# Optimization experiments

Measured on AMD Instinct MI355X. Metric: run time of the kernel, lower is better.

Reference implementation:

```python
import jax, jax.numpy as jnp
import numpy as np

N = 131072          # flattened ray-sample points
C = 32              # output_coordinate_dim per plane
BASE = 128          # base grid resolution
SCALES = [1, 2, 4]  # multiscale_res multipliers
HID = 256           # ResBlock / CondMLP hidden width
OUT = 16            # decoder output dim (geo features)
COMBS = [(0, 1), (0, 2), (1, 2)]  # itertools.combinations(range(3), 2)


def setup_inputs() -> dict:
    key = jax.random.key(0)
    ks = iter(jax.random.split(key, 64))
    inp = {}
    inp['pts'] = jax.random.uniform(next(ks), (N, 3), dtype=jnp.float32)
    inp['aabb'] = jnp.asarray([[0.0, 0.0, 0.0], [1.0, 1.0, 1.0]], dtype=jnp.float32)
    # 9 plane grids: 3 scales x 3 coordinate combinations, uniform in [0.1, 0.5)
    for s, mult in enumerate(SCALES):
        r = BASE * mult
        for ci in range(3):
            inp[f'plane_{s}_{ci}'] = jax.random.uniform(
                next(ks), (C, r, r), dtype=jnp.float32, minval=0.1, maxval=0.5)
    feat_dim = C * len(SCALES)  # concat across scales -> 96
    def lin(k, fin, fout):
        bound = 1.0 / np.sqrt(fin)
        kw, kb = jax.random.split(k)
        w = jax.random.uniform(kw, (fin, fout), dtype=jnp.float32, minval=-bound, maxval=bound)
        b = jax.random.uniform(kb, (fout,), dtype=jnp.float32, minval=-bound, maxval=bound)
        return w, b
    inp['l0_w'], inp['l0_b'] = lin(next(ks), feat_dim, HID)
    # 3 ResBlocks x 3 linears (lz, l1, l2), all 256x256 -> stacked
    rw, rb = [], []
    for _ in range(9):
        w, b = lin(next(ks), HID, HID)
        rw.append(w); rb.append(b)
    inp['res_w'] = jnp.stack(rw).reshape(3, 3, HID, HID)
    inp['res_b'] = jnp.stack(rb).reshape(3, 3, HID)
    inp['l1_w'], inp['l1_b'] = lin(next(ks), HID, OUT)
    return inp


def _bilinear(plane, xy):
    # plane: [C, H, W]; xy: [N, 2] in [-1, 1]; x -> W axis, y -> H axis
    # (F.grid_sample, align_corners=True; border clamp == zeros pad since pts in-bounds)
    Cc, H, W = plane.shape
    x = (xy[:, 0] + 1.0) * 0.5 * (W - 1)
    y = (xy[:, 1] + 1.0) * 0.5 * (H - 1)
    x0 = jnp.clip(jnp.floor(x), 0, W - 2).astype(jnp.int32)
    y0 = jnp.clip(jnp.floor(y), 0, H - 2).astype(jnp.int32)
    x1, y1 = x0 + 1, y0 + 1
    wx = (x - x0)[None, :]
    wy = (y - y0)[None, :]
    v = (plane[:, y0, x0] * (1 - wx) * (1 - wy)
         + plane[:, y0, x1] * wx * (1 - wy)
         + plane[:, y1, x0] * (1 - wx) * wy
         + plane[:, y1, x1] * wx * wy)          # [C, N]
    return v.T                                   # [N, C]


def _interp_ms(xn, planes):
    # planes: list of 3 scales, each a list of 3 [C,H,W] grids
    feats = []
    for scale_planes in planes:
        interp = 1.0
        for plane, (c0, c1) in zip(scale_planes, COMBS):
            xy = jnp.stack([xn[:, c0], xn[:, c1]], axis=-1)
            interp = interp * _bilinear(plane, xy)  # hadamard across planes
        feats.append(interp)
    return jnp.concatenate(feats, axis=-1)          # [N, C*num_scales]


def _cond_mlp(f, l0_w, l0_b, res_w, res_b, l1_w, l1_b):
    x = f @ l0_w + l0_b
    for i in range(3):
        z = jax.nn.relu(x @ res_w[i, 0] + res_b[i, 0])
        res = x + z
        x = jax.nn.relu(res @ res_w[i, 1] + res_b[i, 1])
        x = jax.nn.relu(x @ res_w[i, 2] + res_b[i, 2]) + res
    return jax.nn.sigmoid(x @ l1_w + l1_b)


def reference(pts, aabb,
              plane_0_0, plane_0_1, plane_0_2,
              plane_1_0, plane_1_1, plane_1_2,
              plane_2_0, plane_2_1, plane_2_2,
              l0_w, l0_b, res_w, res_b, l1_w, l1_b):
    xn = (pts - aabb[0]) * (2.0 / (aabb[1] - aabb[0])) - 1.0  # normalize_aabb
    planes = [[plane_0_0, plane_0_1, plane_0_2],
              [plane_1_0, plane_1_1, plane_1_2],
              [plane_2_0, plane_2_1, plane_2_2]]
    feats = _interp_ms(xn, planes)                            # [N, 96]
    return _cond_mlp(feats, l0_w, l0_b, res_w, res_b, l1_w, l1_b)  # [N, 16]
```

## Files before the change

### kernel.cpp

```cpp
#include <hip/hip_runtime.h>

typedef unsigned short u16;
typedef unsigned int u32;
typedef __attribute__((ext_vector_type(2))) unsigned int u32x2;
typedef __attribute__((ext_vector_type(8))) short short8;
typedef __attribute__((ext_vector_type(8))) _Float16 half8;
typedef __attribute__((ext_vector_type(2))) __fp16 fp16x2;
typedef __attribute__((ext_vector_type(4))) float floatx4;

__device__ __forceinline__ u16 f2h(float f){ _Float16 h = (_Float16)f; return __builtin_bit_cast(u16, h); }
__device__ __forceinline__ u32 pkrtz(float a, float b){
  fp16x2 h = __builtin_amdgcn_cvt_pkrtz(a, b);
  return __builtin_bit_cast(u32, h);
}
__device__ __forceinline__ u32 pkmax0(u32 a){
  u32 d, z = 0;
  asm("v_pk_max_f16 %0, %1, %2" : "=v"(d) : "v"(a), "v"(z));
  return d;
}
__device__ __forceinline__ u32 pkadd(u32 a, u32 b){
  u32 d;
  asm("v_pk_add_f16 %0, %1, %2" : "=v"(d) : "v"(a), "v"(b));
  return d;
}

struct PlanePtrs { const void* p[9]; };
struct PtransArgs { const float* src[9]; u16* dst[9]; int blk0[10]; int HW[9]; };

__global__ void ptrans_all_kernel(PtransArgs a){
  __shared__ float tile[32][257];
  int bi = blockIdx.x;
  int i = 0;
  #pragma unroll
  for (int k = 1; k < 9; k++) if (bi >= a.blk0[k]) i = k;
  const float* src = a.src[i];
  u16* dst = a.dst[i];
  const int HW = a.HW[i];
  const int t = threadIdx.x;
  const size_t hw0 = (size_t)(bi - a.blk0[i]) * 256;
  #pragma unroll
  for (int c = 0; c < 32; c++) tile[c][t] = src[(size_t)c*HW + hw0 + t];
  __syncthreads();
  u32* d32 = (u32*)(dst + hw0*32);
  #pragma unroll
  for (int k = 0; k < 16; k++){
    int idx = k*512 + t*2;
    int j = idx >> 5, cc = idx & 31;
    u32 lo = f2h(tile[cc][j]);
    u32 hi = f2h(tile[cc+1][j]);
    d32[k*256 + t] = lo | (hi << 16);
  }
}

__device__ __forceinline__ void wconv_one(const float* src, u16* dst, int fin, int fout, int t){
  int per = fin * fout;
  int m = t / per, r = t - m*per;
  int KS = fin >> 5;
  int e = r & 7;
  int lane = (r >> 3) & 63;
  int fs = r >> 9;
  int ks = fs % KS, ft = fs / KS;
  int of = ft*16 + (lane & 15);
  int k  = ks*32 + (lane >> 4)*8 + e;
  dst[t] = f2h(src[(size_t)m*per + (size_t)k*fout + of]);
}
__global__ void wconv_all_kernel(const float* l0_w, const float* res_w, const float* l1_w,
                                 u16* l0T, u16* resT, u16* l1T){
  int t = blockIdx.x*256 + threadIdx.x;
  if (t < 24576){ wconv_one(l0_w, l0T, 96, 256, t); return; }
  t -= 24576;
  if (t < 589824){ wconv_one(res_w, resT, 256, 256, t); return; }
  t -= 589824;
  if (t < 4096){ wconv_one(l1_w, l1T, 256, 16, t); }
}

__global__ void interp_fb_kernel(const float* __restrict__ pts, const float* __restrict__ aabb,
                                 PlanePtrs pp, u16* __restrict__ feats, int N)
{
  int n = blockIdx.x*256 + threadIdx.x;
  if (n >= N) return;
  float xn[3];
  #pragma unroll
  for (int d=0; d<3; d++){
    float lo = aabb[d], hi = aabb[3+d];
    xn[d] = (pts[(size_t)n*3 + d] - lo) * (2.0f/(hi - lo)) - 1.0f;
  }
  const int c0s[3] = {0,0,1};
  const int c1s[3] = {1,2,2};
  #pragma unroll
  for (int s=0; s<3; s++){
    const int R = 128 << s;
    float prod[32];
    #pragma unroll
    for (int p=0; p<3; p++){
      float fx = (xn[c0s[p]] + 1.0f) * 0.5f * (float)(R-1);
      float fy = (xn[c1s[p]] + 1.0f) * 0.5f * (float)(R-1);
      float fx0 = fminf(fmaxf(floorf(fx), 0.0f), (float)(R-2));
      float fy0 = fminf(fmaxf(floorf(fy), 0.0f), (float)(R-2));
      int x0 = (int)fx0, y0 = (int)fy0;
      float wx = fx - fx0, wy = fy - fy0;
      float w00 = (1.0f-wx)*(1.0f-wy), w01 = wx*(1.0f-wy);
      float w10 = (1.0f-wx)*wy,        w11 = wx*wy;
      const size_t HW = (size_t)R*R;
      const float* b00f = (const float*)pp.p[s*3+p] + (size_t)y0*R + x0;
      #pragma unroll 4
      for (int c=0; c<32; c++){
        const float* q = b00f + (size_t)c*HW;
        float val = q[0]*w00 + q[1]*w01 + q[R]*w10 + q[R+1]*w11;
        prod[c] = (p == 0) ? val : prod[c]*val;
      }
    }
    #pragma unroll
    for (int vv=0; vv<4; vv++){
      short8 pk8;
      #pragma unroll
      for (int e=0; e<8; e++) pk8[e] = (short)f2h(prod[vv*8+e]);
      *(short8*)(feats + (size_t)n*96 + s*32 + vv*8) = pk8;
    }
  }
}

template<int KSTEPS>
__device__ __forceinline__ void mm_tile(const u16* X, const u16* __restrict__ WTs,
                                        int ftbase, int lane, const floatx4 binit[4],
                                        floatx4 acc[4][4])
{
  const int lr = lane & 15, lg = lane >> 4;
  #pragma unroll
  for (int rf=0; rf<4; rf++)
    #pragma unroll
    for (int cf=0; cf<4; cf++)
      acc[rf][cf] = binit[rf];
  #pragma unroll 1
  for (int ks=0; ks<KSTEPS; ks++){
    half8 w[4];
    #pragma unroll
    for (int rf=0; rf<4; rf++)
      w[rf] = *(const half8*)(WTs + ((size_t)((ftbase+rf)*KSTEPS + ks)*64 + lane)*8);
    half8 x[4];
    #pragma unroll
    for (int cf=0; cf<4; cf++){
      int pt = cf*16 + lr;
      int byt = (pt*512 + (ks*32 + lg*8)*2) ^ ((pt & 7) << 4);
      x[cf] = *(const half8*)((const char*)X + byt);
    }
    __builtin_amdgcn_s_setprio(1);
    #pragma unroll
    for (int rf=0; rf<4; rf++)
      #pragma unroll
      for (int cf=0; cf<4; cf++)
        acc[rf][cf] = __builtin_amdgcn_mfma_f32_16x16x32_f16(w[rf], x[cf], acc[rf][cf], 0, 0, 0);
    __builtin_amdgcn_s_setprio(0);
  }
}

__device__ __forceinline__ void load_binit(const float* b, int wb, int lg, floatx4* bi){
  #pragma unroll
  for (int rf=0; rf<4; rf++){
    float4 v = *(const float4*)(b + wb + rf*16 + lg*4);
    bi[rf] = (floatx4){v.x, v.y, v.z, v.w};
  }
}

template<bool GATHER>
__global__ __launch_bounds__(256, 3) void mlp_kernel(
    const float* __restrict__ pts, const float* __restrict__ aabb, PlanePtrs pp,
    const u16* __restrict__ feats,
    const u16* __restrict__ l0T, const u16* __restrict__ resT, const u16* __restrict__ l1T,
    const float* __restrict__ l0_b, const float* __restrict__ res_b, const float* __restrict__ l1_b,
    float* __restrict__ out)
{
  __shared__ u16 X[64*256];
  const int tid = threadIdx.x;
  const int wave = tid >> 6, lane = tid & 63;
  const int lr = lane & 15, lg = lane >> 4;
  const int n0 = blockIdx.x * 64;
  const int ftbase = wave * 4;
  const int wb = wave * 64;

  if constexpr (GATHER){
    const int pt = tid >> 2, v = tid & 3;
    const int n = n0 + pt;
    float xn[3];
    #pragma unroll
    for (int d=0; d<3; d++){
      float lo = aabb[d], hi = aabb[3+d];
      xn[d] = (pts[(size_t)n*3 + d] - lo) * (2.0f/(hi - lo)) - 1.0f;
    }
    const int c0s[3] = {0,0,1};
    const int c1s[3] = {1,2,2};
    #pragma unroll
    for (int s=0; s<3; s++){
      const int R = 128 << s;
      float prod[8];
      #pragma unroll
      for (int p=0; p<3; p++){
        float fx = (xn[c0s[p]] + 1.0f) * 0.5f * (float)(R-1);
        float fy = (xn[c1s[p]] + 1.0f) * 0.5f * (float)(R-1);
        float fx0 = fminf(fmaxf(floorf(fx), 0.0f), (float)(R-2));
        float fy0 = fminf(fmaxf(floorf(fy), 0.0f), (float)(R-2));
        int x0 = (int)fx0, y0 = (int)fy0;
        float wx = fx - fx0, wy = fy - fy0;
        float w00 = (1.0f-wx)*(1.0f-wy), w01 = wx*(1.0f-wy);
        float w10 = (1.0f-wx)*wy,        w11 = wx*wy;
        const u16* base = (const u16*)pp.p[s*3 + p];
        const u16* b00 = base + ((size_t)y0*R + x0)*32 + v*8;
        const u16* b10 = b00 + (size_t)R*32;
        half8 h00 = *(const half8*)b00;
        half8 h01 = *(const half8*)(b00 + 32);
        half8 h10 = *(const half8*)b10;
        half8 h11 = *(const half8*)(b10 + 32);
        #pragma unroll
        for (int e=0; e<8; e++){
          float val = (float)h00[e]*w00 + (float)h01[e]*w01 + (float)h10[e]*w10 + (float)h11[e]*w11;
          prod[e] = (p == 0) ? val : prod[e]*val;
        }
      }
      short8 pk8;
      #pragma unroll
      for (int e=0; e<8; e++) pk8[e] = (short)f2h(prod[e]);
      int byt = (pt*512 + (s*32 + v*8)*2) ^ ((pt & 7) << 4);
      *(short8*)((char*)X + byt) = pk8;
    }
  } else {
    #pragma unroll
    for (int i=0; i<3; i++){
      int id = tid + i*256;
      int row = id / 12, sub = id - row*12;
      short8 v = *(const short8*)(feats + (size_t)(n0+row)*96 + sub*8);
      int byt = (row*512 + sub*16) ^ ((row & 7) << 4);
      *(short8*)((char*)X + byt) = v;
    }
  }
  __syncthreads();

  floatx4 acc[4][4];
  floatx4 binit[4];
  u32 pk[4][4][2];

  load_binit(l0_b, wb, lg, binit);
  mm_tile<3>(X, l0T, ftbase, lane, binit, acc);
  __syncthreads();
  #pragma unroll
  for (int rf=0; rf<4; rf++){
    int fby = (wb + rf*16 + lg*4)*2;
    #pragma unroll
    for (int cf=0; cf<4; cf++){
      int pt = cf*16 + lr;
      u32 p0 = pkrtz(acc[rf][cf][0], acc[rf][cf][1]);
      u32 p1 = pkrtz(acc[rf][cf][2], acc[rf][cf][3]);
      pk[rf][cf][0] = p0; pk[rf][cf][1] = p1;
      int byt = (pt*512 + fby) ^ ((pt & 7) << 4);
      *(u32x2*)((char*)X + byt) = (u32x2){p0, p1};
    }
  }
  __syncthreads();

  for (int rb=0; rb<3; rb++){
    const u16* W0 = resT + (size_t)(rb*3+0)*65536;
    const u16* W1 = resT + (size_t)(rb*3+1)*65536;
    const u16* W2 = resT + (size_t)(rb*3+2)*65536;
    const float* b0 = res_b + (rb*3+0)*256;
    const float* b1 = res_b + (rb*3+1)*256;
    const float* b2 = res_b + (rb*3+2)*256;

    load_binit(b0, wb, lg, binit);
    mm_tile<8>(X, W0, ftbase, lane, binit, acc);
    __syncthreads();
    #pragma unroll
    for (int rf=0; rf<4; rf++){
      int fby = (wb + rf*16 + lg*4)*2;
      #pragma unroll
      for (int cf=0; cf<4; cf++){
        int pt = cf*16 + lr;
        u32 p0 = pkadd(pk[rf][cf][0], pkmax0(pkrtz(acc[rf][cf][0], acc[rf][cf][1])));
        u32 p1 = pkadd(pk[rf][cf][1], pkmax0(pkrtz(acc[rf][cf][2], acc[rf][cf][3])));
        pk[rf][cf][0] = p0; pk[rf][cf][1] = p1;
        int byt = (pt*512 + fby) ^ ((pt & 7) << 4);
        *(u32x2*)((char*)X + byt) = (u32x2){p0, p1};
      }
    }
    __syncthreads();

    load_binit(b1, wb, lg, binit);
    mm_tile<8>(X, W1, ftbase, lane, binit, acc);
    __syncthreads();
    #pragma unroll
    for (int rf=0; rf<4; rf++){
      int fby = (wb + rf*16 + lg*4)*2;
      #pragma unroll
      for (int cf=0; cf<4; cf++){
        int pt = cf*16 + lr;
        u32 p0 = pkmax0(pkrtz(acc[rf][cf][0], acc[rf][cf][1]));
        u32 p1 = pkmax0(pkrtz(acc[rf][cf][2], acc[rf][cf][3]));
        int byt = (pt*512 + fby) ^ ((pt & 7) << 4);
        *(u32x2*)((char*)X + byt) = (u32x2){p0, p1};
      }
    }
    __syncthreads();

    load_binit(b2, wb, lg, binit);
    mm_tile<8>(X, W2, ftbase, lane, binit, acc);
    __syncthreads();
    #pragma unroll
    for (int rf=0; rf<4; rf++){
      int fby = (wb + rf*16 + lg*4)*2;
      #pragma unroll
      for (int cf=0; cf<4; cf++){
        int pt = cf*16 + lr;
        u32 p0 = pkadd(pkmax0(pkrtz(acc[rf][cf][0], acc[rf][cf][1])), pk[rf][cf][0]);
        u32 p1 = pkadd(pkmax0(pkrtz(acc[rf][cf][2], acc[rf][cf][3])), pk[rf][cf][1]);
        pk[rf][cf][0] = p0; pk[rf][cf][1] = p1;
        int byt = (pt*512 + fby) ^ ((pt & 7) << 4);
        *(u32x2*)((char*)X + byt) = (u32x2){p0, p1};
      }
    }
    __syncthreads();
  }

  floatx4 accf;
  {
    float4 bo = *(const float4*)(l1_b + lg*4);
    accf = (floatx4){bo.x, bo.y, bo.z, bo.w};
  }
  #pragma unroll 1
  for (int ks=0; ks<8; ks++){
    int pt = wave*16 + lr;
    int byt = (pt*512 + (ks*32 + lg*8)*2) ^ ((pt&7)<<4);
    half8 x = *(const half8*)((const char*)X + byt);
    half8 w = *(const half8*)(l1T + ((size_t)ks*64 + lane)*8);
    accf = __builtin_amdgcn_mfma_f32_16x16x32_f16(w, x, accf, 0, 0, 0);
  }
  {
    float4 o;
    o.x = 1.0f / (1.0f + __expf(-accf[0]));
    o.y = 1.0f / (1.0f + __expf(-accf[1]));
    o.z = 1.0f / (1.0f + __expf(-accf[2]));
    o.w = 1.0f / (1.0f + __expf(-accf[3]));
    *(float4*)(out + (size_t)(n0 + wave*16 + lr)*16 + lg*4) = o;
  }
}

extern "C" void kernel_launch(void* const* d_in, const int* in_sizes, int n_in,
                              void* d_out, int out_size, void* d_ws, size_t ws_size,
                              hipStream_t stream)
{
  const float* pts  = (const float*)d_in[0];
  const float* aabb = (const float*)d_in[1];
  const float* l0_w = (const float*)d_in[11];
  const float* res_w= (const float*)d_in[13];
  const float* l1_w = (const float*)d_in[15];
  const float* l0_b = (const float*)d_in[12];
  const float* res_b= (const float*)d_in[14];
  const float* l1_b = (const float*)d_in[16];
  const int N = in_sizes[0] / 3;

  char* ws = (char*)d_ws;
  const size_t woff_l0  = 0;
  const size_t woff_res = 49152;
  const size_t woff_l1  = woff_res + 9*65536*2;
  const size_t foff     = woff_l1 + 8192;
  const size_t poff     = foff + (size_t)N*96*2;

  static const int HWs[3] = {128*128, 256*256, 512*512};
  size_t pel[9]; size_t tot = 0;
  for (int s=0;s<3;s++) for (int p=0;p<3;p++){ pel[s*3+p] = tot; tot += (size_t)HWs[s]*32; }

  const bool tr_mode = (ws_size >= poff + tot*2);

  wconv_all_kernel<<<(24576+589824+4096+255)/256, 256, 0, stream>>>(
      l0_w, res_w, l1_w, (u16*)(ws+woff_l0), (u16*)(ws+woff_res), (u16*)(ws+woff_l1));

  PlanePtrs pp;
  if (tr_mode){
    u16* pbase = (u16*)(ws + poff);
    PtransArgs pa;
    int b0 = 0;
    for (int i=0;i<9;i++){
      int s = i/3;
      pa.src[i] = (const float*)d_in[2+i];
      pa.dst[i] = pbase + pel[i];
      pa.blk0[i] = b0;
      pa.HW[i] = HWs[s];
      b0 += HWs[s]/256;
      pp.p[i] = pbase + pel[i];
    }
    pa.blk0[9] = b0;
    ptrans_all_kernel<<<b0, 256, 0, stream>>>(pa);
    mlp_kernel<true><<<N/64, 256, 0, stream>>>(pts, aabb, pp, (const u16*)nullptr,
        (const u16*)(ws+woff_l0), (const u16*)(ws+woff_res), (const u16*)(ws+woff_l1),
        l0_b, res_b, l1_b, (float*)d_out);
  } else {
    for (int i=0;i<9;i++) pp.p[i] = d_in[2+i];
    interp_fb_kernel<<<(N+255)/256, 256, 0, stream>>>(pts, aabb, pp, (u16*)(ws+foff), N);
    mlp_kernel<false><<<N/64, 256, 0, stream>>>(pts, aabb, pp, (const u16*)(ws+foff),
        (const u16*)(ws+woff_l0), (const u16*)(ws+woff_res), (const u16*)(ws+woff_l1),
        l0_b, res_b, l1_b, (float*)d_out);
  }
}
```

Before: 223.9 us.

## Morton-sort points before fused gather-MLP to improve plane gather locality

Adds a counting sort of sample points by a 15-bit Morton key: histogram, scan and scatter kernels. The fused MLP kernel then processes points in spatial order through an index indirection and writes results back to their original positions. The aim is to make the bilinear plane gathers of neighbouring workgroups hit the same cache lines instead of random memory. It also remaps block IDs across the 8 XCDs and widens the LDS XOR swizzle from 3 to 5 bits. In exchange it adds four small launches, global atomics, a single-block scan and scattered output stores.

```diff
diff --git a/kernel.cpp b/kernel.cpp
--- a/kernel.cpp
+++ b/kernel.cpp
@@ -72,6 +72,52 @@
   if (t < 589824){ wconv_one(res_w, resT, 256, 256, t); return; }
   t -= 589824;
   if (t < 4096){ wconv_one(l1_w, l1T, 256, 16, t); }
+}
+
+__device__ __forceinline__ u32 morton_key(const float* __restrict__ pts,
+                                          const float* __restrict__ aabb, int n){
+  u32 key = 0;
+  #pragma unroll
+  for (int d=0; d<3; d++){
+    float lo = aabb[d], hi = aabb[3+d];
+    float xn = (pts[(size_t)n*3 + d] - lo) * (2.0f/(hi - lo)) - 1.0f;
+    int q = (int)((xn + 1.0f) * 16.0f);
+    q = q < 0 ? 0 : (q > 31 ? 31 : q);
+    #pragma unroll
+    for (int b=0; b<5; b++) key |= ((u32)(q >> b) & 1u) << (b*3 + d);
+  }
+  return key;
+}
+__global__ void hist_zero_kernel(u32* hist){ hist[blockIdx.x*256 + threadIdx.x] = 0; }
+__global__ void hist_kernel(const float* pts, const float* aabb, u32* hist, int N){
+  int n = blockIdx.x*256 + threadIdx.x;
+  if (n >= N) return;
+  atomicAdd(&hist[morton_key(pts, aabb, n)], 1u);
+}
+__global__ void scan_kernel(u32* hist){
+  __shared__ u32 sums[1024];
+  int t = threadIdx.x;
+  u32 local[32]; u32 s = 0;
+  #pragma unroll
+  for (int i=0; i<32; i++){ local[i] = hist[t*32 + i]; s += local[i]; }
+  sums[t] = s;
+  __syncthreads();
+  for (int off=1; off<1024; off<<=1){
+    u32 v = (t >= off) ? sums[t-off] : 0;
+    __syncthreads();
+    sums[t] += v;
+    __syncthreads();
+  }
+  u32 base = (t == 0) ? 0 : sums[t-1];
+  #pragma unroll
+  for (int i=0; i<32; i++){ u32 c = local[i]; hist[t*32 + i] = base; base += c; }
+}
+__global__ void scatter_kernel(const float* pts, const float* aabb, u32* hist,
+                               int* sidx, int N){
+  int n = blockIdx.x*256 + threadIdx.x;
+  if (n >= N) return;
+  u32 pos = atomicAdd(&hist[morton_key(pts, aabb, n)], 1u);
+  sidx[pos] = n;
 }
 
 __global__ void interp_fb_kernel(const float* __restrict__ pts, const float* __restrict__ aabb,
@@ -141,7 +187,7 @@
     #pragma unroll
     for (int cf=0; cf<4; cf++){
       int pt = cf*16 + lr;
-      int byt = (pt*512 + (ks*32 + lg*8)*2) ^ ((pt & 7) << 4);
+      int byt = (pt*512 + (ks*32 + lg*8)*2) ^ ((pt & 31) << 4);
       x[cf] = *(const half8*)((const char*)X + byt);
     }
     __builtin_amdgcn_s_setprio(1);
@@ -162,10 +208,10 @@
   }
 }
 
-template<bool GATHER>
+template<int MODE>
 __global__ __launch_bounds__(256, 3) void mlp_kernel(
     const float* __restrict__ pts, const float* __restrict__ aabb, PlanePtrs pp,
-    const u16* __restrict__ feats,
+    const u16* __restrict__ feats, const int* __restrict__ sidx,
     const u16* __restrict__ l0T, const u16* __restrict__ resT, const u16* __restrict__ l1T,
     const float* __restrict__ l0_b, const float* __restrict__ res_b, const float* __restrict__ l1_b,
     float* __restrict__ out)
@@ -174,13 +220,18 @@
   const int tid = threadIdx.x;
   const int wave = tid >> 6, lane = tid & 63;
   const int lr = lane & 15, lg = lane >> 4;
-  const int n0 = blockIdx.x * 64;
+  int bid = blockIdx.x;
+  if constexpr (MODE == 2){
+    int nwg = gridDim.x;
+    if ((nwg & 7) == 0) bid = (bid & 7)*(nwg >> 3) + (bid >> 3);
+  }
+  const int n0 = bid * 64;
   const int ftbase = wave * 4;
   const int wb = wave * 64;
 
-  if constexpr (GATHER){
+  if constexpr (MODE >= 1){
     const int pt = tid >> 2, v = tid & 3;
-    const int n = n0 + pt;
+    const int n = (MODE == 2) ? sidx[n0 + pt] : (n0 + pt);
     float xn[3];
     #pragma unroll
     for (int d=0; d<3; d++){
@@ -219,7 +270,7 @@
       short8 pk8;
       #pragma unroll
       for (int e=0; e<8; e++) pk8[e] = (short)f2h(prod[e]);
-      int byt = (pt*512 + (s*32 + v*8)*2) ^ ((pt & 7) << 4);
+      int byt = (pt*512 + (s*32 + v*8)*2) ^ ((pt & 31) << 4);
       *(short8*)((char*)X + byt) = pk8;
     }
   } else {
@@ -228,7 +279,7 @@
       int id = tid + i*256;
       int row = id / 12, sub = id - row*12;
       short8 v = *(const short8*)(feats + (size_t)(n0+row)*96 + sub*8);
-      int byt = (row*512 + sub*16) ^ ((row & 7) << 4);
+      int byt = (row*512 + sub*16) ^ ((row & 31) << 4);
       *(short8*)((char*)X + byt) = v;
     }
   }
@@ -250,7 +301,7 @@
       u32 p0 = pkrtz(acc[rf][cf][0], acc[rf][cf][1]);
       u32 p1 = pkrtz(acc[rf][cf][2], acc[rf][cf][3]);
       pk[rf][cf][0] = p0; pk[rf][cf][1] = p1;
-      int byt = (pt*512 + fby) ^ ((pt & 7) << 4);
+      int byt = (pt*512 + fby) ^ ((pt & 31) << 4);
       *(u32x2*)((char*)X + byt) = (u32x2){p0, p1};
     }
   }
@@ -276,7 +327,7 @@
         u32 p0 = pkadd(pk[rf][cf][0], pkmax0(pkrtz(acc[rf][cf][0], acc[rf][cf][1])));
         u32 p1 = pkadd(pk[rf][cf][1], pkmax0(pkrtz(acc[rf][cf][2], acc[rf][cf][3])));
         pk[rf][cf][0] = p0; pk[rf][cf][1] = p1;
-        int byt = (pt*512 + fby) ^ ((pt & 7) << 4);
+        int byt = (pt*512 + fby) ^ ((pt & 31) << 4);
         *(u32x2*)((char*)X + byt) = (u32x2){p0, p1};
       }
     }
@@ -293,7 +344,7 @@
         int pt = cf*16 + lr;
         u32 p0 = pkmax0(pkrtz(acc[rf][cf][0], acc[rf][cf][1]));
         u32 p1 = pkmax0(pkrtz(acc[rf][cf][2], acc[rf][cf][3]));
-        int byt = (pt*512 + fby) ^ ((pt & 7) << 4);
+        int byt = (pt*512 + fby) ^ ((pt & 31) << 4);
         *(u32x2*)((char*)X + byt) = (u32x2){p0, p1};
       }
     }
@@ -311,7 +362,7 @@
         u32 p0 = pkadd(pkmax0(pkrtz(acc[rf][cf][0], acc[rf][cf][1])), pk[rf][cf][0]);
         u32 p1 = pkadd(pkmax0(pkrtz(acc[rf][cf][2], acc[rf][cf][3])), pk[rf][cf][1]);
         pk[rf][cf][0] = p0; pk[rf][cf][1] = p1;
-        int byt = (pt*512 + fby) ^ ((pt & 7) << 4);
+        int byt = (pt*512 + fby) ^ ((pt & 31) << 4);
         *(u32x2*)((char*)X + byt) = (u32x2){p0, p1};
       }
     }
@@ -326,18 +377,20 @@
   #pragma unroll 1
   for (int ks=0; ks<8; ks++){
     int pt = wave*16 + lr;
-    int byt = (pt*512 + (ks*32 + lg*8)*2) ^ ((pt&7)<<4);
+    int byt = (pt*512 + (ks*32 + lg*8)*2) ^ ((pt&31)<<4);
     half8 x = *(const half8*)((const char*)X + byt);
     half8 w = *(const half8*)(l1T + ((size_t)ks*64 + lane)*8);
     accf = __builtin_amdgcn_mfma_f32_16x16x32_f16(w, x, accf, 0, 0, 0);
   }
   {
+    int li = n0 + wave*16 + lr;
+    int n_out = (MODE == 2) ? sidx[li] : li;
     float4 o;
     o.x = 1.0f / (1.0f + __expf(-accf[0]));
     o.y = 1.0f / (1.0f + __expf(-accf[1]));
     o.z = 1.0f / (1.0f + __expf(-accf[2]));
     o.w = 1.0f / (1.0f + __expf(-accf[3]));
-    *(float4*)(out + (size_t)(n0 + wave*16 + lr)*16 + lg*4) = o;
+    *(float4*)(out + (size_t)n_out*16 + lg*4) = o;
   }
 }
 
@@ -366,7 +419,10 @@
   size_t pel[9]; size_t tot = 0;
   for (int s=0;s<3;s++) for (int p=0;p<3;p++){ pel[s*3+p] = tot; tot += (size_t)HWs[s]*32; }
 
-  const bool tr_mode = (ws_size >= poff + tot*2);
+  const size_t hoff = (poff + tot*2 + 255) & ~(size_t)255;
+  const size_t ioff = hoff + 32768*4;
+  const bool tr_mode   = (ws_size >= poff + tot*2);
+  const bool sort_mode = (ws_size >= ioff + (size_t)N*4) && ((N/64) % 8 == 0) && (N % 256 == 0);
 
   wconv_all_kernel<<<(24576+589824+4096+255)/256, 256, 0, stream>>>(
       l0_w, res_w, l1_w, (u16*)(ws+woff_l0), (u16*)(ws+woff_res), (u16*)(ws+woff_l1));
@@ -387,13 +443,26 @@
     }
     pa.blk0[9] = b0;
     ptrans_all_kernel<<<b0, 256, 0, stream>>>(pa);
-    mlp_kernel<true><<<N/64, 256, 0, stream>>>(pts, aabb, pp, (const u16*)nullptr,
-        (const u16*)(ws+woff_l0), (const u16*)(ws+woff_res), (const u16*)(ws+woff_l1),
-        l0_b, res_b, l1_b, (float*)d_out);
+
+    if (sort_mode){
+      u32* hist = (u32*)(ws + hoff);
+      int* sidx = (int*)(ws + ioff);
+      hist_zero_kernel<<<128, 256, 0, stream>>>(hist);
+      hist_kernel<<<(N+255)/256, 256, 0, stream>>>(pts, aabb, hist, N);
+      scan_kernel<<<1, 1024, 0, stream>>>(hist);
+      scatter_kernel<<<(N+255)/256, 256, 0, stream>>>(pts, aabb, hist, sidx, N);
+      mlp_kernel<2><<<N/64, 256, 0, stream>>>(pts, aabb, pp, (const u16*)nullptr, sidx,
+          (const u16*)(ws+woff_l0), (const u16*)(ws+woff_res), (const u16*)(ws+woff_l1),
+          l0_b, res_b, l1_b, (float*)d_out);
+    } else {
+      mlp_kernel<1><<<N/64, 256, 0, stream>>>(pts, aabb, pp, (const u16*)nullptr, (const int*)nullptr,
+          (const u16*)(ws+woff_l0), (const u16*)(ws+woff_res), (const u16*)(ws+woff_l1),
+          l0_b, res_b, l1_b, (float*)d_out);
+    }
   } else {
     for (int i=0;i<9;i++) pp.p[i] = d_in[2+i];
     interp_fb_kernel<<<(N+255)/256, 256, 0, stream>>>(pts, aabb, pp, (u16*)(ws+foff), N);
-    mlp_kernel<false><<<N/64, 256, 0, stream>>>(pts, aabb, pp, (const u16*)(ws+foff),
+    mlp_kernel<0><<<N/64, 256, 0, stream>>>(pts, aabb, pp, (const u16*)(ws+foff), (const int*)nullptr,
         (const u16*)(ws+woff_l0), (const u16*)(ws+woff_res), (const u16*)(ws+woff_l1),
         l0_b, res_b, l1_b, (float*)d_out);
   }
```

New measurement: 234.8 us. +4.9%, slower.
